# Kernel optimization log

Measured on AMD Instinct MI355X. Metric: run time of the kernel, lower is better.

## Reference

```python
import jax, jax.numpy as jnp
import numpy as np
import math

N_LAYERS = 8
D = 1024
H = 16
DK = D // H
T = 1024
V = 32000
B = 2
DFF = 4 * D
EPS = 1e-5


def layernorm(x, scale, bias):
    mu = jnp.mean(x, axis=-1, keepdims=True)
    var = jnp.mean(jnp.square(x - mu), axis=-1, keepdims=True)
    return (x - mu) * jax.lax.rsqrt(var + EPS) * scale + bias


def setup_inputs() -> dict:
    key = jax.random.key(0)
    ks = jax.random.split(key, 32)
    s = 0.02
    rn = lambda k, shape: jax.random.normal(k, shape, dtype=jnp.float32) * s
    x = jax.random.randint(ks[0], (B, T), 0, V)
    return {
        "x": x,
        "inp_emb": rn(ks[1], (V, D)),
        "pos_emb": rn(ks[2], (T, D)),
        # per-layer weights stacked on leading layer axis; per-head wq/wk/wv are
        # concatenated along the output dim (mathematically identical to the
        # per-head nn.Linear list in the torch code)
        "wq": rn(ks[3], (N_LAYERS, D, D)), "bq": jnp.zeros((N_LAYERS, D), jnp.float32),
        "wk": rn(ks[4], (N_LAYERS, D, D)), "bk": jnp.zeros((N_LAYERS, D), jnp.float32),
        "wv": rn(ks[5], (N_LAYERS, D, D)), "bv": jnp.zeros((N_LAYERS, D), jnp.float32),
        "wo": rn(ks[6], (N_LAYERS, D, D)), "bo": jnp.zeros((N_LAYERS, D), jnp.float32),
        "w1": rn(ks[7], (N_LAYERS, D, DFF)), "b1": jnp.zeros((N_LAYERS, DFF), jnp.float32),
        "w2": rn(ks[8], (N_LAYERS, DFF, D)), "b2": jnp.zeros((N_LAYERS, D), jnp.float32),
        "ln1_s": jnp.ones((N_LAYERS, D), jnp.float32), "ln1_b": jnp.zeros((N_LAYERS, D), jnp.float32),
        "ln2_s": jnp.ones((N_LAYERS, D), jnp.float32), "ln2_b": jnp.zeros((N_LAYERS, D), jnp.float32),
        "lno_s": jnp.ones((D,), jnp.float32), "lno_b": jnp.zeros((D,), jnp.float32),
        "w_out": rn(ks[9], (D, V)),
    }


def reference(x, inp_emb, pos_emb, wq, bq, wk, bk, wv, bv, wo, bo,
              w1, b1, w2, b2, ln1_s, ln1_b, ln2_s, ln2_b, lno_s, lno_b, w_out):
    h = inp_emb[x] + pos_emb[jnp.arange(T)]            # [B,T,D]
    causal = jnp.tril(jnp.ones((T, T), dtype=bool))    # [T,T]
    scale = 1.0 / math.sqrt(DK)
    for i in range(N_LAYERS):
        # --- multi-head causal attention ---
        xn = layernorm(h, ln1_s[i], ln1_b[i])
        q = (xn @ wq[i] + bq[i]).reshape(B, T, H, DK)
        k = (xn @ wk[i] + bk[i]).reshape(B, T, H, DK)
        v = (xn @ wv[i] + bv[i]).reshape(B, T, H, DK)
        scores = jnp.einsum('bqhd,bkhd->bhqk', q, k) * scale
        scores = jnp.where(causal, scores, -jnp.inf)
        att = jax.nn.softmax(scores, axis=-1)           # [B,H,T,T]
        y = jnp.einsum('bhqk,bkhd->bqhd', att, v).reshape(B, T, D)
        h = h + y @ wo[i] + bo[i]
        # --- feed-forward ---
        xn = layernorm(h, ln2_s[i], ln2_b[i])
        h = h + jax.nn.gelu(xn @ w1[i] + b1[i], approximate=False) @ w2[i] + b2[i]
    h = layernorm(h, lno_s, lno_b)
    return h @ w_out                                    # logits [B,T,V]
```

## Files before the change

### kernel.cpp

```cpp
#include <hip/hip_runtime.h>
#include <cmath>

#define D_MODEL 1024
#define N_HEADS 16
#define DKH     64
#define SEQ_T   1024
#define BATCH   2
#define VOCAB   32000
#define DFF_    4096
#define NLAYERS 8

typedef __bf16 bf16x8 __attribute__((ext_vector_type(8)));
typedef __bf16 bf16x4v __attribute__((ext_vector_type(4)));
typedef float  f32x4  __attribute__((ext_vector_type(4)));

__device__ __forceinline__ float gelu_f(float x) {
    return 0.5f * x * (1.0f + erff(x * 0.70710678118654752f));
}

__device__ __forceinline__ void gload_lds16(const void* g, void* l) {
    __builtin_amdgcn_global_load_lds(
        (const __attribute__((address_space(1))) void*)g,
        (__attribute__((address_space(3))) void*)l, 16, 0, 0);
}

__global__ __launch_bounds__(256) void embed_kernel(
    const int* __restrict__ x, const float* __restrict__ inp_emb,
    const float* __restrict__ pos_emb, float* __restrict__ h)
{
    const int idx = blockIdx.x * 256 + threadIdx.x;
    const int bt  = idx >> 10;
    const int d   = idx & 1023;
    const int t   = bt & (SEQ_T - 1);
    const int tok = x[bt];
    h[idx] = inp_emb[(size_t)tok * D_MODEL + d] + pos_emb[(size_t)t * D_MODEL + d];
}

__global__ __launch_bounds__(256) void layernorm_kernel(
    const float* __restrict__ x, const float* __restrict__ sc,
    const float* __restrict__ bi, __bf16* __restrict__ o)
{
    const int row = blockIdx.x;
    const int tid = threadIdx.x;
    const int c   = tid * 4;
    const float4 v = *(const float4*)(x + (size_t)row * D_MODEL + c);
    float sum = v.x + v.y + v.z + v.w;
    float sq  = v.x * v.x + v.y * v.y + v.z * v.z + v.w * v.w;
    #pragma unroll
    for (int off = 32; off > 0; off >>= 1) {
        sum += __shfl_xor(sum, off);
        sq  += __shfl_xor(sq, off);
    }
    __shared__ float ssum[4], ssq[4];
    const int wave = tid >> 6, lane = tid & 63;
    if (lane == 0) { ssum[wave] = sum; ssq[wave] = sq; }
    __syncthreads();
    sum = ssum[0] + ssum[1] + ssum[2] + ssum[3];
    sq  = ssq[0]  + ssq[1]  + ssq[2]  + ssq[3];
    const float mu  = sum * (1.0f / D_MODEL);
    const float var = sq * (1.0f / D_MODEL) - mu * mu;
    const float rs  = rsqrtf(var + 1e-5f);
    const float4 s4 = *(const float4*)(sc + c);
    const float4 b4 = *(const float4*)(bi + c);
    bf16x4v ov;
    ov[0] = (__bf16)((v.x - mu) * rs * s4.x + b4.x);
    ov[1] = (__bf16)((v.y - mu) * rs * s4.y + b4.y);
    ov[2] = (__bf16)((v.z - mu) * rs * s4.z + b4.z);
    ov[3] = (__bf16)((v.w - mu) * rs * s4.w + b4.w);
    *(bf16x4v*)(o + (size_t)row * D_MODEL + c) = ov;
}

__global__ __launch_bounds__(256) void prep_layer_kernel(
    const float* __restrict__ wq, const float* __restrict__ wk,
    const float* __restrict__ wv, const float* __restrict__ wo,
    const float* __restrict__ w1, const float* __restrict__ w2,
    const float* __restrict__ bq, const float* __restrict__ bk,
    const float* __restrict__ bv,
    __bf16* __restrict__ wqkvT, __bf16* __restrict__ woT,
    __bf16* __restrict__ w1T, __bf16* __restrict__ w2T,
    float* __restrict__ bqkv)
{
    __shared__ __bf16 tile[32][36];
    const int b   = blockIdx.x;
    const int tid = threadIdx.x;

    if (b >= 12288) {
        const int j = (b - 12288) * 256 + tid;
        bqkv[j] = (j < 1024) ? bq[j] : (j < 2048 ? bk[j - 1024] : bv[j - 2048]);
        return;
    }

    const float* in;
    __bf16* out;
    int K, N, kb0, nb0;
    if (b < 4096) {
        const int w = b >> 10, t = b & 1023;
        K = 1024; N = 1024; kb0 = (t >> 5) * 32; nb0 = (t & 31) * 32;
        in  = (w == 0) ? wq : (w == 1) ? wk : (w == 2) ? wv : wo;
        out = (w == 3) ? woT : wqkvT + (size_t)w * 1024 * 1024;
    } else if (b < 8192) {
        const int t = b - 4096;
        K = 1024; N = 4096; kb0 = (t >> 7) * 32; nb0 = (t & 127) * 32;
        in = w1; out = w1T;
    } else {
        const int t = b - 8192;
        K = 4096; N = 1024; kb0 = (t >> 5) * 32; nb0 = (t & 31) * 32;
        in = w2; out = w2T;
    }

    {
        const int rr = tid >> 3, c4 = (tid & 7) * 4;
        const float4 v = *(const float4*)(in + (size_t)(kb0 + rr) * N + nb0 + c4);
        tile[rr][c4 + 0] = (__bf16)v.x;
        tile[rr][c4 + 1] = (__bf16)v.y;
        tile[rr][c4 + 2] = (__bf16)v.z;
        tile[rr][c4 + 3] = (__bf16)v.w;
    }
    __syncthreads();
    {
        const int cc = tid >> 3, r4 = (tid & 7) * 4;
        bf16x4v ov;
        ov[0] = tile[r4 + 0][cc];
        ov[1] = tile[r4 + 1][cc];
        ov[2] = tile[r4 + 2][cc];
        ov[3] = tile[r4 + 3][cc];
        *(bf16x4v*)(out + (size_t)(nb0 + cc) * K + kb0 + r4) = ov;
    }
}

__global__ __launch_bounds__(256) void wout_tr_kernel(
    const float* __restrict__ in, __bf16* __restrict__ out)
{
    __shared__ __bf16 tile[32][36];
    const int tid = threadIdx.x;
    const int nb0 = (blockIdx.x >> 5) * 32;
    const int kb0 = (blockIdx.x & 31) * 32;
    {
        const int rr = tid >> 3, c4 = (tid & 7) * 4;
        const float4 v = *(const float4*)(in + (size_t)(kb0 + rr) * VOCAB + nb0 + c4);
        tile[rr][c4 + 0] = (__bf16)v.x;
        tile[rr][c4 + 1] = (__bf16)v.y;
        tile[rr][c4 + 2] = (__bf16)v.z;
        tile[rr][c4 + 3] = (__bf16)v.w;
    }
    __syncthreads();
    {
        const int cc = tid >> 3, r4 = (tid & 7) * 4;
        bf16x4v ov;
        ov[0] = tile[r4 + 0][cc];
        ov[1] = tile[r4 + 1][cc];
        ov[2] = tile[r4 + 2][cc];
        ov[3] = tile[r4 + 3][cc];
        *(bf16x4v*)(out + (size_t)(nb0 + cc) * D_MODEL + kb0 + r4) = ov;
    }
}

template <int BN_T, int EPI, typename OutT, bool NT = false>
__global__ __launch_bounds__(256) void gemm_bt(
    const __bf16* __restrict__ A, const __bf16* __restrict__ Bt,
    const float* __restrict__ bias, const float* __restrict__ res,
    OutT* __restrict__ C, int M, int N, int K)
{
    constexpr int NF  = BN_T / 32;
    constexpr int NCB = BN_T / 8;
    __shared__ __bf16 As[128 * 64];
    __shared__ __bf16 Bs[BN_T * 64];

    const int tid  = threadIdx.x;
    const int wave = tid >> 6;
    const int lane = tid & 63;
    const int r    = lane & 15;
    const int kb   = lane >> 4;
    const int wm   = wave >> 1;
    const int wn   = wave & 1;

    const int ntm = gridDim.x;
    const int nwg = ntm * gridDim.y;
    int bid = blockIdx.y * ntm + blockIdx.x;
    if ((nwg & 7) == 0) bid = (bid & 7) * (nwg >> 3) + (bid >> 3);
    const int bm = (bid % ntm) * 128;
    const int bn = (bid / ntm) * BN_T;

    const int srow = lane >> 3;
    const int sg   = lane & 7;

    f32x4 acc[4][NF] = {};

    for (int k0 = 0; k0 < K; k0 += 64) {
        #pragma unroll
        for (int i = 0; i < 4; ++i) {
            const int c    = i * 4 + wave;
            const int row  = c * 8 + srow;
            const int scol = (sg ^ (row & 7)) * 8;
            gload_lds16(A + (size_t)(bm + row) * K + k0 + scol, &As[c * 512]);
        }
        #pragma unroll
        for (int i = 0; i < NCB / 4; ++i) {
            const int c    = i * 4 + wave;
            const int row  = c * 8 + srow;
            const int scol = (sg ^ (row & 7)) * 8;
            gload_lds16(Bt + (size_t)(bn + row) * K + k0 + scol, &Bs[c * 512]);
        }
        __syncthreads();

        #pragma unroll
        for (int s = 0; s < 2; ++s) {
            bf16x8 af[4];
            #pragma unroll
            for (int m = 0; m < 4; ++m) {
                const int row = wm * 64 + m * 16 + r;
                const int g   = (s * 4 + kb) ^ (row & 7);
                af[m] = *(const bf16x8*)&As[row * 64 + g * 8];
            }
            #pragma unroll
            for (int n = 0; n < NF; ++n) {
                const int row = wn * (NF * 16) + n * 16 + r;
                const int g   = (s * 4 + kb) ^ (row & 7);
                const bf16x8 bfr = *(const bf16x8*)&Bs[row * 64 + g * 8];
                #pragma unroll
                for (int m = 0; m < 4; ++m)
                    acc[m][n] = __builtin_amdgcn_mfma_f32_16x16x32_bf16(af[m], bfr, acc[m][n], 0, 0, 0);
            }
        }
        __syncthreads();
    }

    #pragma unroll
    for (int m = 0; m < 4; ++m) {
        const int row = bm + wm * 64 + m * 16 + kb * 4;
        #pragma unroll
        for (int n = 0; n < NF; ++n) {
            const int col = bn + wn * (NF * 16) + n * 16 + r;
            const float bv = bias ? bias[col] : 0.0f;
            #pragma unroll
            for (int rg = 0; rg < 4; ++rg) {
                float v = acc[m][n][rg] + bv;
                if constexpr (EPI == 1) v += res[(size_t)(row + rg) * N + col];
                if constexpr (EPI == 2) v = gelu_f(v);
                if constexpr (NT) {
                    __builtin_nontemporal_store((OutT)v, &C[(size_t)(row + rg) * N + col]);
                } else {
                    C[(size_t)(row + rg) * N + col] = (OutT)v;
                }
            }
        }
    }
}

struct AttnState {
    float m[4];
    float l[4];
    f32x4 yacc[4];
};

__device__ __forceinline__ void attn_tile_step(
    AttnState& st, const bf16x8 (&qf)[2], int q0, int kt,
    int wave, int r, int kb,
    const __bf16 (*K_lds)[72], const __bf16 (*V_lds)[72],
    __bf16 (*P_row)[72])
{
    f32x4 sacc[4] = {};
    #pragma unroll
    for (int kc = 0; kc < 2; ++kc) {
        #pragma unroll
        for (int g = 0; g < 4; ++g) {
            const bf16x8 kf = *(const bf16x8*)&K_lds[g * 16 + r][kc * 32 + kb * 8];
            sacc[g] = __builtin_amdgcn_mfma_f32_16x16x32_bf16(qf[kc], kf, sacc[g], 0, 0, 0);
        }
    }

    float s[4][4], p[4][4];
    #pragma unroll
    for (int g = 0; g < 4; ++g) {
        const int key = kt * 64 + g * 16 + r;
        #pragma unroll
        for (int rg = 0; rg < 4; ++rg) {
            const int qq = q0 + wave * 16 + kb * 4 + rg;
            s[g][rg] = (key <= qq) ? sacc[g][rg] * 0.125f : -INFINITY;
        }
    }
    float mt[4], mn[4], corr[4], psum[4];
    #pragma unroll
    for (int rg = 0; rg < 4; ++rg)
        mt[rg] = fmaxf(fmaxf(s[0][rg], s[1][rg]), fmaxf(s[2][rg], s[3][rg]));
    #pragma unroll
    for (int off = 1; off < 16; off <<= 1) {
        #pragma unroll
        for (int rg = 0; rg < 4; ++rg) mt[rg] = fmaxf(mt[rg], __shfl_xor(mt[rg], off));
    }
    #pragma unroll
    for (int rg = 0; rg < 4; ++rg) {
        mn[rg]  = fmaxf(st.m[rg], mt[rg]);
        psum[rg] = 0.0f;
        #pragma unroll
        for (int g = 0; g < 4; ++g) {
            p[g][rg] = __expf(s[g][rg] - mn[rg]);
            psum[rg] += p[g][rg];
        }
    }
    #pragma unroll
    for (int off = 1; off < 16; off <<= 1) {
        #pragma unroll
        for (int rg = 0; rg < 4; ++rg) psum[rg] += __shfl_xor(psum[rg], off);
    }
    #pragma unroll
    for (int rg = 0; rg < 4; ++rg) {
        corr[rg] = __expf(st.m[rg] - mn[rg]);
        st.l[rg] = st.l[rg] * corr[rg] + psum[rg];
        st.m[rg] = mn[rg];
    }
    #pragma unroll
    for (int n = 0; n < 4; ++n) {
        #pragma unroll
        for (int rg = 0; rg < 4; ++rg) st.yacc[n][rg] *= corr[rg];
    }

    #pragma unroll
    for (int g = 0; g < 4; ++g) {
        #pragma unroll
        for (int rg = 0; rg < 4; ++rg)
            P_row[kb * 4 + rg][g * 16 + r] = (__bf16)p[g][rg];
    }
    const bf16x8 pa0 = *(const bf16x8*)&P_row[r][kb * 8];
    const bf16x8 pa1 = *(const bf16x8*)&P_row[r][32 + kb * 8];

    #pragma unroll
    for (int n = 0; n < 4; ++n) {
        const int vrow = n * 16 + r;
        const int swz  = (vrow >> 3) & 7;
        const bf16x8 vf0 = *(const bf16x8*)&V_lds[vrow][(kb ^ swz) * 8];
        st.yacc[n] = __builtin_amdgcn_mfma_f32_16x16x32_bf16(pa0, vf0, st.yacc[n], 0, 0, 0);
    }
    #pragma unroll
    for (int n = 0; n < 4; ++n) {
        const int vrow = n * 16 + r;
        const int swz  = (vrow >> 3) & 7;
        const bf16x8 vf1 = *(const bf16x8*)&V_lds[vrow][((kb + 4) ^ swz) * 8];
        st.yacc[n] = __builtin_amdgcn_mfma_f32_16x16x32_bf16(pa1, vf1, st.yacc[n], 0, 0, 0);
    }
}

__global__ __launch_bounds__(256) void attn_mfma_kernel(
    const __bf16* __restrict__ qkv, __bf16* __restrict__ y)
{
    constexpr int QS = 3 * D_MODEL;
    __shared__ __align__(16) __bf16 K_lds[64][72];
    __shared__ __align__(16) __bf16 V_lds[64][72];
    __shared__ __align__(16) __bf16 P_lds[4][16][72];

    const int tid  = threadIdx.x;
    const int wave = tid >> 6;
    const int lane = tid & 63;
    const int r    = lane & 15;
    const int kb   = lane >> 4;

    const int ip  = blockIdx.x;
    const int q0A = ip * 64;
    const int q0B = (15 - ip) * 64;
    const int b   = blockIdx.y >> 4;
    const int h   = blockIdx.y & 15;

    const __bf16* qp = qkv + (size_t)b * SEQ_T * QS + h * DKH;
    const __bf16* kp = qp + D_MODEL;
    const __bf16* vp = qp + 2 * D_MODEL;
    __bf16* yp = y + (size_t)b * SEQ_T * D_MODEL + h * DKH;

    bf16x8 qfA[2], qfB[2];
    {
        const int qrA = q0A + wave * 16 + r;
        const int qrB = q0B + wave * 16 + r;
        #pragma unroll
        for (int kc = 0; kc < 2; ++kc) {
            qfA[kc] = *(const bf16x8*)(qp + (size_t)qrA * QS + kc * 32 + kb * 8);
            qfB[kc] = *(const bf16x8*)(qp + (size_t)qrB * QS + kc * 32 + kb * 8);
        }
    }

    AttnState stA, stB;
    #pragma unroll
    for (int rg = 0; rg < 4; ++rg) {
        stA.m[rg] = -INFINITY; stA.l[rg] = 0.0f;
        stB.m[rg] = -INFINITY; stB.l[rg] = 0.0f;
    }
    #pragma unroll
    for (int n = 0; n < 4; ++n) { stA.yacc[n] = {}; stB.yacc[n] = {}; }

    const int skey = tid >> 2;
    const int sg16 = (tid & 3) * 16;

    const int ntiles = 16 - ip;
    for (int kt = 0; kt < ntiles; ++kt) {
        {
            const size_t go = (size_t)(kt * 64 + skey) * QS;
            *(bf16x8*)&K_lds[skey][sg16]     = *(const bf16x8*)(kp + go + sg16);
            *(bf16x8*)&K_lds[skey][sg16 + 8] = *(const bf16x8*)(kp + go + sg16 + 8);
            const bf16x8 v0 = *(const bf16x8*)(vp + go + sg16);
            const bf16x8 v1 = *(const bf16x8*)(vp + go + sg16 + 8);
            const int swz0 = ((sg16 >> 3) & 7) * 8;
            const int swz1 = (((sg16 + 8) >> 3) & 7) * 8;
            #pragma unroll
            for (int j = 0; j < 8; ++j)
                V_lds[sg16 + j][skey ^ swz0] = v0[j];
            #pragma unroll
            for (int j = 0; j < 8; ++j)
                V_lds[sg16 + 8 + j][skey ^ swz1] = v1[j];
        }
        __syncthreads();

        attn_tile_step(stB, qfB, q0B, kt, wave, r, kb, K_lds, V_lds, P_lds[wave]);
        if (kt <= ip)
            attn_tile_step(stA, qfA, q0A, kt, wave, r, kb, K_lds, V_lds, P_lds[wave]);
        __syncthreads();
    }

    float invA[4], invB[4];
    #pragma unroll
    for (int rg = 0; rg < 4; ++rg) {
        invA[rg] = 1.0f / stA.l[rg];
        invB[rg] = 1.0f / stB.l[rg];
    }
    #pragma unroll
    for (int n = 0; n < 4; ++n) {
        #pragma unroll
        for (int rg = 0; rg < 4; ++rg) {
            const int rowA = q0A + wave * 16 + kb * 4 + rg;
            const int rowB = q0B + wave * 16 + kb * 4 + rg;
            yp[(size_t)rowA * D_MODEL + n * 16 + r] = (__bf16)(stA.yacc[n][rg] * invA[rg]);
            yp[(size_t)rowB * D_MODEL + n * 16 + r] = (__bf16)(stB.yacc[n][rg] * invB[rg]);
        }
    }
}

extern "C" void kernel_launch(void* const* d_in, const int* in_sizes, int n_in,
                              void* d_out, int out_size, void* d_ws, size_t ws_size,
                              hipStream_t stream)
{
    const int*   x       = (const int*)  d_in[0];
    const float* inp_emb = (const float*)d_in[1];
    const float* pos_emb = (const float*)d_in[2];
    const float* wq = (const float*)d_in[3];
    const float* bq = (const float*)d_in[4];
    const float* wk = (const float*)d_in[5];
    const float* bk = (const float*)d_in[6];
    const float* wv = (const float*)d_in[7];
    const float* bv = (const float*)d_in[8];
    const float* wo = (const float*)d_in[9];
    const float* bo = (const float*)d_in[10];
    const float* w1 = (const float*)d_in[11];
    const float* b1 = (const float*)d_in[12];
    const float* w2 = (const float*)d_in[13];
    const float* b2 = (const float*)d_in[14];
    const float* ln1_s = (const float*)d_in[15];
    const float* ln1_b = (const float*)d_in[16];
    const float* ln2_s = (const float*)d_in[17];
    const float* ln2_b = (const float*)d_in[18];
    const float* lno_s = (const float*)d_in[19];
    const float* lno_b = (const float*)d_in[20];
    const float* w_out = (const float*)d_in[21];

    const int M = BATCH * SEQ_T;
    const size_t MB = 1u << 20;

    char* w = (char*)d_ws;
    float*  h     = (float*) (w + 0);
    __bf16* xn    = (__bf16*)(w + 8  * MB);
    __bf16* yb    = (__bf16*)(w + 12 * MB);
    __bf16* sh    = (__bf16*)(w + 16 * MB);
    __bf16* wqkvT = (__bf16*)(w + 32 * MB);
    __bf16* woT   = (__bf16*)(w + 38 * MB);
    __bf16* w1T   = (__bf16*)(w + 40 * MB);
    __bf16* w2T   = (__bf16*)(w + 48 * MB);
    float*  bqkv  = (float*) (w + 56 * MB);
    __bf16* woutT = (__bf16*)(w + 57 * MB);

    embed_kernel<<<dim3(M * D_MODEL / 256), 256, 0, stream>>>(x, inp_emb, pos_emb, h);

    for (int i = 0; i < NLAYERS; ++i) {
        const size_t wOff  = (size_t)i * D_MODEL * D_MODEL;
        const size_t w1Off = (size_t)i * D_MODEL * DFF_;

        prep_layer_kernel<<<dim3(12300), 256, 0, stream>>>(
            wq + wOff, wk + wOff, wv + wOff, wo + wOff, w1 + w1Off, w2 + w1Off,
            bq + i * D_MODEL, bk + i * D_MODEL, bv + i * D_MODEL,
            wqkvT, woT, w1T, w2T, bqkv);

        layernorm_kernel<<<dim3(M), 256, 0, stream>>>(h, ln1_s + i * D_MODEL, ln1_b + i * D_MODEL, xn);
        gemm_bt<128, 0, __bf16><<<dim3(M / 128, 3 * D_MODEL / 128), 256, 0, stream>>>(
            xn, wqkvT, bqkv, nullptr, sh, M, 3 * D_MODEL, D_MODEL);
        attn_mfma_kernel<<<dim3(8, BATCH * N_HEADS), 256, 0, stream>>>(sh, yb);
        gemm_bt<64, 1, float><<<dim3(M / 128, D_MODEL / 64), 256, 0, stream>>>(
            yb, woT, bo + i * D_MODEL, h, h, M, D_MODEL, D_MODEL);
        layernorm_kernel<<<dim3(M), 256, 0, stream>>>(h, ln2_s + i * D_MODEL, ln2_b + i * D_MODEL, xn);
        gemm_bt<128, 2, __bf16><<<dim3(M / 128, DFF_ / 128), 256, 0, stream>>>(
            xn, w1T, b1 + i * DFF_, nullptr, sh, M, DFF_, D_MODEL);
        gemm_bt<64, 1, float><<<dim3(M / 128, D_MODEL / 64), 256, 0, stream>>>(
            sh, w2T, b2 + i * D_MODEL, h, h, M, D_MODEL, DFF_);
    }

    wout_tr_kernel<<<dim3((VOCAB / 32) * 32), 256, 0, stream>>>(w_out, woutT);
    layernorm_kernel<<<dim3(M), 256, 0, stream>>>(h, lno_s, lno_b, xn);
    gemm_bt<128, 0, float, true><<<dim3(M / 128, VOCAB / 128), 256, 0, stream>>>(
        xn, woutT, nullptr, nullptr, (float*)d_out, M, VOCAB, D_MODEL);
}
```

Before: 1.712 ms.

## Skip causal mask off-diagonal, lazily rescale softmax, shrink QKV GEMM tile

Templates the attention tile step on whether causal masking is needed, applying the mask only on diagonal tiles. Replaces the per-tile online-softmax correction with a conditional rescale that fires only when the row max grows by more than a threshold, avoiding exps and accumulator multiplies on most tiles. Also halves the N tile of the QKV projection GEMM to launch more blocks. The lazy rescale lets unnormalized probabilities reach larger magnitudes before bf16 conversion, a small numeric risk.

Measured after the change: 1.675 ms. 2.2% less time.

```diff
diff --git a/kernel.cpp b/kernel.cpp
--- a/kernel.cpp
+++ b/kernel.cpp
@@ -253,6 +253,7 @@
     f32x4 yacc[4];
 };
 
+template <bool MASK>
 __device__ __forceinline__ void attn_tile_step(
     AttnState& st, const bf16x8 (&qf)[2], int q0, int kt,
     int wave, int r, int kb,
@@ -272,14 +273,19 @@
     float s[4][4], p[4][4];
     #pragma unroll
     for (int g = 0; g < 4; ++g) {
-        const int key = kt * 64 + g * 16 + r;
         #pragma unroll
         for (int rg = 0; rg < 4; ++rg) {
-            const int qq = q0 + wave * 16 + kb * 4 + rg;
-            s[g][rg] = (key <= qq) ? sacc[g][rg] * 0.125f : -INFINITY;
-        }
-    }
-    float mt[4], mn[4], corr[4], psum[4];
+            if constexpr (MASK) {
+                const int key = kt * 64 + g * 16 + r;
+                const int qq  = q0 + wave * 16 + kb * 4 + rg;
+                s[g][rg] = (key <= qq) ? sacc[g][rg] * 0.125f : -INFINITY;
+            } else {
+                s[g][rg] = sacc[g][rg] * 0.125f;
+            }
+        }
+    }
+
+    float mt[4];
     #pragma unroll
     for (int rg = 0; rg < 4; ++rg)
         mt[rg] = fmaxf(fmaxf(s[0][rg], s[1][rg]), fmaxf(s[2][rg], s[3][rg]));
@@ -288,13 +294,29 @@
         #pragma unroll
         for (int rg = 0; rg < 4; ++rg) mt[rg] = fmaxf(mt[rg], __shfl_xor(mt[rg], off));
     }
+
+    bool grow = false;
+    #pragma unroll
+    for (int rg = 0; rg < 4; ++rg) grow |= (mt[rg] > st.m[rg] + 8.0f);
+    if (__any(grow)) {
+        #pragma unroll
+        for (int rg = 0; rg < 4; ++rg) {
+            const float mn   = fmaxf(st.m[rg], mt[rg]);
+            const float corr = __expf(st.m[rg] - mn);
+            st.l[rg] *= corr;
+            st.m[rg]  = mn;
+            #pragma unroll
+            for (int n = 0; n < 4; ++n) st.yacc[n][rg] *= corr;
+        }
+    }
+
+    float psum[4];
     #pragma unroll
     for (int rg = 0; rg < 4; ++rg) {
-        mn[rg]  = fmaxf(st.m[rg], mt[rg]);
         psum[rg] = 0.0f;
         #pragma unroll
         for (int g = 0; g < 4; ++g) {
-            p[g][rg] = __expf(s[g][rg] - mn[rg]);
+            p[g][rg] = __expf(s[g][rg] - st.m[rg]);
             psum[rg] += p[g][rg];
         }
     }
@@ -304,16 +326,7 @@
         for (int rg = 0; rg < 4; ++rg) psum[rg] += __shfl_xor(psum[rg], off);
     }
     #pragma unroll
-    for (int rg = 0; rg < 4; ++rg) {
-        corr[rg] = __expf(st.m[rg] - mn[rg]);
-        st.l[rg] = st.l[rg] * corr[rg] + psum[rg];
-        st.m[rg] = mn[rg];
-    }
-    #pragma unroll
-    for (int n = 0; n < 4; ++n) {
-        #pragma unroll
-        for (int rg = 0; rg < 4; ++rg) st.yacc[n][rg] *= corr[rg];
-    }
+    for (int rg = 0; rg < 4; ++rg) st.l[rg] += psum[rg];
 
     #pragma unroll
     for (int g = 0; g < 4; ++g) {
@@ -407,9 +420,16 @@
         }
         __syncthreads();
 
-        attn_tile_step(stB, qfB, q0B, kt, wave, r, kb, K_lds, V_lds, P_lds[wave]);
-        if (kt <= ip)
-            attn_tile_step(stA, qfA, q0A, kt, wave, r, kb, K_lds, V_lds, P_lds[wave]);
+        if (kt == ntiles - 1)
+            attn_tile_step<true >(stB, qfB, q0B, kt, wave, r, kb, K_lds, V_lds, P_lds[wave]);
+        else
+            attn_tile_step<false>(stB, qfB, q0B, kt, wave, r, kb, K_lds, V_lds, P_lds[wave]);
+        if (kt <= ip) {
+            if (kt == ip)
+                attn_tile_step<true >(stA, qfA, q0A, kt, wave, r, kb, K_lds, V_lds, P_lds[wave]);
+            else
+                attn_tile_step<false>(stA, qfA, q0A, kt, wave, r, kb, K_lds, V_lds, P_lds[wave]);
+        }
         __syncthreads();
     }
 
@@ -485,7 +505,7 @@
             wqkvT, woT, w1T, w2T, bqkv);
 
         layernorm_kernel<<<dim3(M), 256, 0, stream>>>(h, ln1_s + i * D_MODEL, ln1_b + i * D_MODEL, xn);
-        gemm_bt<128, 0, __bf16><<<dim3(M / 128, 3 * D_MODEL / 128), 256, 0, stream>>>(
+        gemm_bt<64, 0, __bf16><<<dim3(M / 128, 3 * D_MODEL / 64), 256, 0, stream>>>(
             xn, wqkvT, bqkv, nullptr, sh, M, 3 * D_MODEL, D_MODEL);
         attn_mfma_kernel<<<dim3(8, BATCH * N_HEADS), 256, 0, stream>>>(sh, yb);
         gemm_bt<64, 1, float><<<dim3(M / 128, D_MODEL / 64), 256, 0, stream>>>(
```
